# Kernel optimization log

Measured on AMD Instinct MI355X. Metric: run time of the kernel, lower is better.

The kernel has to match this reference:

```python
import jax, jax.numpy as jnp
import numpy as np

B, S, N, H, K = 8, 4096, 2048, 768, 50


def setup_inputs() -> dict:
    key = jax.random.key(0)
    ks = jax.random.split(key, 6)
    sequence_output = jax.random.normal(ks[0], (B, S, H), jnp.float32)
    span_starts = jnp.sort(jax.random.randint(ks[1], (B, N), 0, S - 8), axis=-1)
    span_lengths = jax.random.randint(ks[2], (B, N), 0, 8)  # extra tokens beyond start
    entity_anchor = jax.random.uniform(ks[3], (3, H), jnp.float32, -1.0, 1.0)
    relation_embeddings = jax.random.uniform(ks[4], (4, 2 * H), jnp.float32, -1.0, 1.0)
    nota_embeddings = jax.random.uniform(ks[5], (20, 2 * H), jnp.float32, -1.0, 1.0)
    return dict(sequence_output=sequence_output, span_starts=span_starts,
                span_lengths=span_lengths, entity_anchor=entity_anchor,
                relation_embeddings=relation_embeddings, nota_embeddings=nota_embeddings)


def reference(sequence_output, span_starts, span_lengths, entity_anchor,
              relation_embeddings, nota_embeddings):
    # --- ragged span MEAN pooling via prefix sums (vectorized over all spans) ---
    # P[b, i] = sum of tokens < i ; shape [B, S+1, H]
    P = jnp.concatenate(
        [jnp.zeros_like(sequence_output[:, :1]), jnp.cumsum(sequence_output, axis=1)], axis=1)
    n_tok = span_lengths + 1                       # tokens per span, in [1, 8]
    end_exc = span_starts + n_tok                  # exclusive end index
    gather = lambda idx: jnp.take_along_axis(P, idx[..., None], axis=1)
    span_sum = gather(end_exc) - gather(span_starts)          # [B, N, H]
    embs = span_sum / n_tok[..., None].astype(span_sum.dtype) # [B, N, H]

    # --- span scoring against entity anchors, top-k mention selection ---
    span_scores = jnp.einsum('bnh,ch->bnc', embs, entity_anchor)  # [B, N, 3]
    span_scores_max = span_scores.max(axis=-1)                    # [B, N]
    _, top_idx = jax.lax.top_k(span_scores_max, K)                # [B, K]
    sel = jnp.take_along_axis(embs, top_idx[..., None], axis=1)   # [B, K, H]

    # --- pairwise (h, t) relation scoring. cat(h,t) . W == h . W_h + t . W_t,
    # so we avoid materializing the [B,K,K,2H] pair tensor. ---
    Wr_h, Wr_t = relation_embeddings[:, :H], relation_embeddings[:, H:]
    Wn_h, Wn_t = nota_embeddings[:, :H], nota_embeddings[:, H:]
    rel = (jnp.einsum('bkh,rh->bkr', sel, Wr_h)[:, :, None, :]
           + jnp.einsum('bkh,rh->bkr', sel, Wr_t)[:, None, :, :])   # [B, K, K, 4]
    nota = (jnp.einsum('bkh,mh->bkm', sel, Wn_h)[:, :, None, :]
            + jnp.einsum('bkh,mh->bkm', sel, Wn_t)[:, None, :, :])  # [B, K, K, 20]
    nota_max = nota.max(axis=-1, keepdims=True)                     # [B, K, K, 1]
    return jnp.concatenate([nota_max, rel], axis=-1)                # [B, K, K, 5]
```

## Files before the change

### kernel.cpp

```cpp
#include <hip/hip_runtime.h>
#include <cstdint>
#include <cstddef>

#define NB 8
#define NS 4096
#define NN 2048
#define NH 768
#define NK 50

__global__ __launch_bounds__(256) void kd_rowdots(const float* __restrict__ x,
                                                  const float* __restrict__ anchor,
                                                  float* __restrict__ rowdot) {
  const int lane = threadIdx.x & 63;
  const int gw   = blockIdx.x * 4 + (threadIdx.x >> 6);

  float4 a[3][3];
#pragma unroll
  for (int c = 0; c < 3; ++c)
#pragma unroll
    for (int p = 0; p < 3; ++p)
      a[c][p] = *reinterpret_cast<const float4*>(anchor + c * NH + p * 256 + lane * 4);

  const float* base = x + (size_t)gw * 8 * NH + lane * 4;

  float4 va[3], vb[3];
#pragma unroll
  for (int p = 0; p < 3; ++p)
    va[p] = *reinterpret_cast<const float4*>(base + p * 256);

#define KD_LOAD(V, I)                                                         \
  {                                                                           \
    const float* s_ = base + (size_t)(I) * NH;                                \
    _Pragma("unroll")                                                         \
    for (int p = 0; p < 3; ++p)                                               \
      V[p] = *reinterpret_cast<const float4*>(s_ + p * 256);                  \
  }
#define KD_CONS(V, I)                                                         \
  {                                                                           \
    float d0 = 0.f, d1 = 0.f, d2 = 0.f;                                       \
    _Pragma("unroll")                                                         \
    for (int p = 0; p < 3; ++p) {                                             \
      d0 += V[p].x * a[0][p].x + V[p].y * a[0][p].y +                         \
            V[p].z * a[0][p].z + V[p].w * a[0][p].w;                          \
      d1 += V[p].x * a[1][p].x + V[p].y * a[1][p].y +                         \
            V[p].z * a[1][p].z + V[p].w * a[1][p].w;                          \
      d2 += V[p].x * a[2][p].x + V[p].y * a[2][p].y +                         \
            V[p].z * a[2][p].z + V[p].w * a[2][p].w;                          \
    }                                                                         \
    _Pragma("unroll")                                                         \
    for (int o = 32; o > 0; o >>= 1) {                                        \
      d0 += __shfl_xor(d0, o);                                                \
      d1 += __shfl_xor(d1, o);                                                \
      d2 += __shfl_xor(d2, o);                                                \
    }                                                                         \
    if (lane == 0) {                                                          \
      int r = gw * 8 + (I);                                                   \
      float* o_ = rowdot + (size_t)r * 3;                                     \
      o_[0] = d0; o_[1] = d1; o_[2] = d2;                                     \
    }                                                                         \
  }

#pragma unroll
  for (int i = 0; i < 8; i += 2) {
    KD_LOAD(vb, i + 1)
    KD_CONS(va, i)
    if (i + 2 < 8) KD_LOAD(va, i + 2)
    KD_CONS(vb, i + 1)
  }
#undef KD_LOAD
#undef KD_CONS
}

__global__ __launch_bounds__(1024) void k3f_topk(const float* __restrict__ rowdot,
                                                 const int* __restrict__ starts,
                                                 const int* __restrict__ lens,
                                                 int* __restrict__ topidx) {
  const int b    = blockIdx.x;
  const int tid  = threadIdx.x;
  const int lane = tid & 63;

  __shared__ unsigned cnt[16][4];
  __shared__ unsigned long long cand[NN];
  __shared__ unsigned candcnt;

  if (tid < 64) cnt[tid >> 2][tid & 3] = 0u;
  if (tid == 64) candcnt = 0u;

  unsigned long long key0, key1;
#pragma unroll
  for (int half = 0; half < 2; ++half) {
    const int sp = tid + half * 1024;
    const int st = starts[b * NN + sp];
    const int n  = lens[b * NN + sp] + 1;
    const float* rd = rowdot + ((size_t)b * NS + st) * 3;
    float v0[8], v1[8], v2[8];
#pragma unroll
    for (int r = 0; r < 8; ++r) {
      v0[r] = rd[r * 3];
      v1[r] = rd[r * 3 + 1];
      v2[r] = rd[r * 3 + 2];
    }
    float s0 = 0.f, s1 = 0.f, s2 = 0.f;
#pragma unroll
    for (int r = 0; r < 8; ++r) {
      const bool c = r < n;
      const float t0 = s0 + v0[r], t1 = s1 + v1[r], t2 = s2 + v2[r];
      s0 = c ? t0 : s0; s1 = c ? t1 : s1; s2 = c ? t2 : s2;
    }
    float sc = fmaxf(s0, fmaxf(s1, s2)) / (float)n;
    unsigned u   = __float_as_uint(sc);
    unsigned ord = (u & 0x80000000u) ? ~u : (u | 0x80000000u);
    unsigned long long k = ((unsigned long long)ord << 32) | (unsigned)(NN - 1 - sp);
    if (half == 0) key0 = k; else key1 = k;
  }
  const unsigned ord0 = (unsigned)(key0 >> 32);
  const unsigned ord1 = (unsigned)(key1 >> 32);
  __syncthreads();

  unsigned T = 0;
  int rem = NK;
  bool a0 = true, a1 = true;
#pragma unroll
  for (int it = 0; it < 16; ++it) {
    const int bit = 30 - 2 * it;
    const int u0 = a0 ? (int)((ord0 >> bit) & 3) : -1;
    const int u1 = a1 ? (int)((ord1 >> bit) & 3) : -1;
    const unsigned c3 = __popcll(__ballot(u0 == 3)) + __popcll(__ballot(u1 == 3));
    const unsigned c2 = __popcll(__ballot(u0 == 2)) + __popcll(__ballot(u1 == 2));
    const unsigned c1 = __popcll(__ballot(u0 == 1)) + __popcll(__ballot(u1 == 1));
    if (lane == 0) {
      if (c3) atomicAdd(&cnt[it][3], c3);
      if (c2) atomicAdd(&cnt[it][2], c2);
      if (c1) atomicAdd(&cnt[it][1], c1);
    }
    __syncthreads();
    const int C3 = (int)cnt[it][3];
    const int C2 = (int)cnt[it][2];
    const int C1 = (int)cnt[it][1];
    int d;
    if (C3 >= rem)                 d = 3;
    else if (C3 + C2 >= rem)      { d = 2; rem -= C3; }
    else if (C3 + C2 + C1 >= rem) { d = 1; rem -= C3 + C2; }
    else                          { d = 0; rem -= C3 + C2 + C1; }
    T |= ((unsigned)d) << bit;
    a0 = a0 && (u0 == d);
    a1 = a1 && (u1 == d);
  }

  if (ord0 >= T) { unsigned p = atomicAdd(&candcnt, 1u); cand[p] = key0; }
  if (ord1 >= T) { unsigned p = atomicAdd(&candcnt, 1u); cand[p] = key1; }
  __syncthreads();
  const int M = (int)candcnt;
  for (int i = tid; i < M; i += 1024) {
    const unsigned long long ki = cand[i];
    int r = 0;
    for (int j = 0; j < M; ++j) r += (cand[j] > ki);
    if (r < NK)
      topidx[b * NK + r] = (NN - 1) - (int)(ki & 0xFFFFFFFFull);
  }
}

__global__ __launch_bounds__(256) void k4a_proj(const float* __restrict__ x,
                                                const int* __restrict__ starts,
                                                const int* __restrict__ lens,
                                                const int* __restrict__ topidx,
                                                const float* __restrict__ rel,
                                                const float* __restrict__ nota,
                                                float* __restrict__ proj) {
  const int blk  = blockIdx.x;
  const int wid  = threadIdx.x >> 6;
  const int lane = threadIdx.x & 63;
  const int b = blk / NK, k = blk % NK;
  const int n  = topidx[b * NK + k];
  const int st = starts[b * NN + n];
  const int nt = lens[b * NN + n] + 1;
  const float fnt = (float)nt;

  float4 e[3];
#pragma unroll
  for (int p = 0; p < 3; ++p) { e[p].x = 0.f; e[p].y = 0.f; e[p].z = 0.f; e[p].w = 0.f; }
  for (int r = 0; r < nt; ++r) {
    const float* row = x + ((size_t)b * NS + st + r) * NH + lane * 4;
#pragma unroll
    for (int p = 0; p < 3; ++p) {
      float4 v = *reinterpret_cast<const float4*>(row + p * 256);
      e[p].x += v.x; e[p].y += v.y; e[p].z += v.z; e[p].w += v.w;
    }
  }
#pragma unroll
  for (int p = 0; p < 3; ++p) {
    e[p].x /= fnt; e[p].y /= fnt; e[p].z /= fnt; e[p].w /= fnt;
  }

#pragma unroll
  for (int j = 0; j < 12; ++j) {
    const int w = wid * 12 + j;
    const float* wr;
    if (w < 4)       wr = rel  + (size_t)w * (2 * NH);
    else if (w < 8)  wr = rel  + (size_t)(w - 4) * (2 * NH) + NH;
    else if (w < 28) wr = nota + (size_t)(w - 8) * (2 * NH);
    else             wr = nota + (size_t)(w - 28) * (2 * NH) + NH;
    wr += lane * 4;
    float d = 0.f;
#pragma unroll
    for (int p = 0; p < 3; ++p) {
      float4 wv = *reinterpret_cast<const float4*>(wr + p * 256);
      d += e[p].x * wv.x + e[p].y * wv.y + e[p].z * wv.z + e[p].w * wv.w;
    }
#pragma unroll
    for (int o = 32; o > 0; o >>= 1) d += __shfl_xor(d, o);
    if (lane == 0) proj[((size_t)b * NK + k) * 48 + w] = d;
  }
}

__global__ __launch_bounds__(256) void k4b_out(const float* __restrict__ proj,
                                               float* __restrict__ out) {
  int idx = blockIdx.x * 256 + threadIdx.x;
  if (idx >= NB * NK * NK) return;
  int b  = idx / (NK * NK);
  int rr = idx % (NK * NK);
  int k1 = rr / NK, k2 = rr % NK;
  const float* p1 = proj + ((size_t)b * NK + k1) * 48;
  const float* p2 = proj + ((size_t)b * NK + k2) * 48;
  float mx = p1[8] + p2[28];
#pragma unroll
  for (int m = 1; m < 20; ++m) mx = fmaxf(mx, p1[8 + m] + p2[28 + m]);
  float* o = out + (size_t)idx * 5;
  o[0] = mx;
#pragma unroll
  for (int r = 0; r < 4; ++r) o[1 + r] = p1[r] + p2[4 + r];
}

extern "C" void kernel_launch(void* const* d_in, const int* in_sizes, int n_in,
                              void* d_out, int out_size, void* d_ws, size_t ws_size,
                              hipStream_t stream) {
  const float* x      = (const float*)d_in[0];
  const int*   starts = (const int*)d_in[1];
  const int*   lens   = (const int*)d_in[2];
  const float* anchor = (const float*)d_in[3];
  const float* rel    = (const float*)d_in[4];
  const float* nota   = (const float*)d_in[5];
  float* out = (float*)d_out;

  char* ws = (char*)d_ws;
  float* rowdot = (float*)ws;
  int*   topidx = (int*)(ws + (size_t)NB * 3 * NS * sizeof(float));
  float* proj   = (float*)(ws + (size_t)NB * 3 * NS * sizeof(float) + 4096);

  hipLaunchKernelGGL(kd_rowdots, dim3(1024), dim3(256), 0, stream, x, anchor, rowdot);
  hipLaunchKernelGGL(k3f_topk, dim3(NB), dim3(1024), 0, stream,
                     rowdot, starts, lens, topidx);
  hipLaunchKernelGGL(k4a_proj, dim3(NB * NK), dim3(256), 0, stream,
                     x, starts, lens, topidx, rel, nota, proj);
  hipLaunchKernelGGL(k4b_out, dim3((NB * NK * NK + 255) / 256), dim3(256), 0, stream,
                     proj, out);
}
```

Measured before the change: 42.97 us.

## Deepen rowdot load pipeline to four buffers and cut radix-select passes

The row-dot kernel now issues four rows of loads up front and keeps four buffers in flight instead of double buffering, so more global loads are outstanding to hide memory latency at the cost of more registers. The top-k kernel's 2-bit radix selection loop is cut from 16 to 8 iterations, which resolves only the top 16 bits of the ordered score key. Any remaining ties are presumably handled by the unseen candidate-collection code, which saves barriers and shared-memory atomics but risks more candidates or incorrect selection if that path does not fully break ties.

```diff
diff --git a/kernel.cpp b/kernel.cpp
--- a/kernel.cpp
+++ b/kernel.cpp
@@ -23,29 +23,26 @@
 
   const float* base = x + (size_t)gw * 8 * NH + lane * 4;
 
-  float4 va[3], vb[3];
-#pragma unroll
-  for (int p = 0; p < 3; ++p)
-    va[p] = *reinterpret_cast<const float4*>(base + p * 256);
-
-#define KD_LOAD(V, I)                                                         \
+  float4 v[4][3];
+
+#define KD_LOAD(B, I)                                                         \
   {                                                                           \
     const float* s_ = base + (size_t)(I) * NH;                                \
     _Pragma("unroll")                                                         \
     for (int p = 0; p < 3; ++p)                                               \
-      V[p] = *reinterpret_cast<const float4*>(s_ + p * 256);                  \
-  }
-#define KD_CONS(V, I)                                                         \
+      v[B][p] = *reinterpret_cast<const float4*>(s_ + p * 256);               \
+  }
+#define KD_CONS(B, I)                                                         \
   {                                                                           \
     float d0 = 0.f, d1 = 0.f, d2 = 0.f;                                       \
     _Pragma("unroll")                                                         \
     for (int p = 0; p < 3; ++p) {                                             \
-      d0 += V[p].x * a[0][p].x + V[p].y * a[0][p].y +                         \
-            V[p].z * a[0][p].z + V[p].w * a[0][p].w;                          \
-      d1 += V[p].x * a[1][p].x + V[p].y * a[1][p].y +                         \
-            V[p].z * a[1][p].z + V[p].w * a[1][p].w;                          \
-      d2 += V[p].x * a[2][p].x + V[p].y * a[2][p].y +                         \
-            V[p].z * a[2][p].z + V[p].w * a[2][p].w;                          \
+      d0 += v[B][p].x * a[0][p].x + v[B][p].y * a[0][p].y +                   \
+            v[B][p].z * a[0][p].z + v[B][p].w * a[0][p].w;                    \
+      d1 += v[B][p].x * a[1][p].x + v[B][p].y * a[1][p].y +                   \
+            v[B][p].z * a[1][p].z + v[B][p].w * a[1][p].w;                    \
+      d2 += v[B][p].x * a[2][p].x + v[B][p].y * a[2][p].y +                   \
+            v[B][p].z * a[2][p].z + v[B][p].w * a[2][p].w;                    \
     }                                                                         \
     _Pragma("unroll")                                                         \
     for (int o = 32; o > 0; o >>= 1) {                                        \
@@ -60,13 +57,15 @@
     }                                                                         \
   }
 
-#pragma unroll
-  for (int i = 0; i < 8; i += 2) {
-    KD_LOAD(vb, i + 1)
-    KD_CONS(va, i)
-    if (i + 2 < 8) KD_LOAD(va, i + 2)
-    KD_CONS(vb, i + 1)
-  }
+  KD_LOAD(0, 0) KD_LOAD(1, 1) KD_LOAD(2, 2) KD_LOAD(3, 3)
+  KD_CONS(0, 0) KD_LOAD(0, 4)
+  KD_CONS(1, 1) KD_LOAD(1, 5)
+  KD_CONS(2, 2) KD_LOAD(2, 6)
+  KD_CONS(3, 3) KD_LOAD(3, 7)
+  KD_CONS(0, 4)
+  KD_CONS(1, 5)
+  KD_CONS(2, 6)
+  KD_CONS(3, 7)
 #undef KD_LOAD
 #undef KD_CONS
 }
@@ -79,12 +78,12 @@
   const int tid  = threadIdx.x;
   const int lane = tid & 63;
 
-  __shared__ unsigned cnt[16][4];
+  __shared__ unsigned cnt[8][4];
   __shared__ unsigned long long cand[NN];
   __shared__ unsigned candcnt;
 
-  if (tid < 64) cnt[tid >> 2][tid & 3] = 0u;
-  if (tid == 64) candcnt = 0u;
+  if (tid < 32) cnt[tid >> 2][tid & 3] = 0u;
+  if (tid == 32) candcnt = 0u;
 
   unsigned long long key0, key1;
 #pragma unroll
@@ -121,7 +120,7 @@
   int rem = NK;
   bool a0 = true, a1 = true;
 #pragma unroll
-  for (int it = 0; it < 16; ++it) {
+  for (int it = 0; it < 8; ++it) {
     const int bit = 30 - 2 * it;
     const int u0 = a0 ? (int)((ord0 >> bit) & 3) : -1;
     const int u1 = a1 ? (int)((ord1 >> bit) & 3) : -1;
```

Measured after the change: 40.54 us (median of 2 runs). 5.7% less time.
